# Performance work log

Hardware: AMD Instinct MI355X
Metric: run time of the kernel (lower is better)

The kernel has to match this reference:

```python
import jax, jax.numpy as jnp
import numpy as np

V, D, H, L, F, B, S = 512, 512, 8, 6, 2048, 8, 1024
DK = D // H
EPS = 1e-5


def _positional_encoding(max_len, d_model):
    pos = np.arange(max_len, dtype=np.float32)[:, None]
    div = np.exp(np.arange(0, d_model, 2, dtype=np.float32) * (-np.log(10000.0) / d_model))
    pe = np.zeros((max_len, d_model), dtype=np.float32)
    pe[:, 0::2] = np.sin(pos * div)
    pe[:, 1::2] = np.cos(pos * div)
    return jnp.asarray(pe)


def setup_inputs() -> dict:
    key = jax.random.key(0)
    ks = jax.random.split(key, 24)
    xavier = lambda k, shp: jax.random.normal(k, shp, jnp.float32) * np.sqrt(2.0 / (shp[-2] + shp[-1]))
    inp = {
        "input_ids": jax.random.randint(ks[0], (B, S), 0, V),
        "emb": jax.random.normal(ks[1], (V, D), jnp.float32) * 0.02,
        "pe": _positional_encoding(1024, D),
        "Wq": xavier(ks[2], (L, D, D)), "bq": jnp.zeros((L, D)),
        "Wk": xavier(ks[3], (L, D, D)), "bk": jnp.zeros((L, D)),
        "Wv": xavier(ks[4], (L, D, D)), "bv": jnp.zeros((L, D)),
        "Wo": xavier(ks[5], (L, D, D)), "bo": jnp.zeros((L, D)),
        "ln1_g": jnp.ones((L, D)), "ln1_b": jnp.zeros((L, D)),
        "W1": xavier(ks[6], (L, D, F)), "b1": jnp.zeros((L, F)),
        "W2": xavier(ks[7], (L, F, D)), "b2": jnp.zeros((L, D)),
        "ln2_g": jnp.ones((L, D)), "ln2_b": jnp.zeros((L, D)),
        "Wout": xavier(ks[8], (D, V)), "bout": jnp.zeros((V,)),
    }
    return inp


def _ln(x, g, b):
    mu = jnp.mean(x, -1, keepdims=True)
    var = jnp.mean(jnp.square(x - mu), -1, keepdims=True)
    return (x - mu) * jax.lax.rsqrt(var + EPS) * g + b


def reference(input_ids, emb, pe, Wq, bq, Wk, bk, Wv, bv, Wo, bo,
              ln1_g, ln1_b, W1, b1, W2, b2, ln2_g, ln2_b, Wout, bout):
    h = emb[input_ids] * np.sqrt(D) + pe[:S]  # [B,S,D]
    # Faithful to the original mask bug: masked_fill(mask==0, -1e9) fills the
    # LOWER triangle (incl diagonal); raw scores are kept strictly where j > i.
    r = jnp.arange(S)
    keep = r[None, :] > r[:, None]  # [S,S]

    def block(h, p):
        (wq, bq_, wk, bk_, wv, bv_, wo, bo_,
         g1, be1, w1, b1_, w2, b2_, g2, be2) = p
        split = lambda t: t.reshape(B, S, H, DK).transpose(0, 2, 1, 3)
        q = split(h @ wq + bq_)
        k = split(h @ wk + bk_)
        v = split(h @ wv + bv_)
        scores = jnp.einsum('bhqd,bhkd->bhqk', q, k) / np.sqrt(DK)
        scores = jnp.where(keep, scores, -1e9)
        a = jax.nn.softmax(scores, axis=-1)
        o = jnp.einsum('bhqk,bhkd->bhqd', a, v).transpose(0, 2, 1, 3).reshape(B, S, D)
        h = _ln(h + (o @ wo + bo_), g1, be1)
        f = jax.nn.relu(h @ w1 + b1_) @ w2 + b2_
        h = _ln(h + f, g2, be2)
        return h, None

    params = (Wq, bq, Wk, bk, Wv, bv, Wo, bo, ln1_g, ln1_b, W1, b1, W2, b2, ln2_g, ln2_b)
    h, _ = jax.lax.scan(block, h, params)
    return h @ Wout + bout  # logits [B,S,V]
```

## Files before the change

### kernel.cpp

```cpp
#include <hip/hip_runtime.h>

typedef unsigned short u16;
typedef __attribute__((ext_vector_type(8))) short bf16x8;
typedef __attribute__((ext_vector_type(4))) float f32x4;
typedef __attribute__((ext_vector_type(4))) unsigned int uint4v;
typedef __attribute__((ext_vector_type(4))) unsigned short us4;

#define NLAYER 6
#define D_MODEL 512
#define NHEAD 8
#define DKH 64
#define SEQ 1024
#define BATCH 8
#define FFN 2048
#define MROWS (BATCH * SEQ)
#define QKV_LD 1536
#define SCALE_LOG2E 0.18033688011112042f

__device__ __forceinline__ float b2f(u16 u) {
  union { unsigned u32; float f; } x; x.u32 = ((unsigned)u) << 16; return x.f;
}
__device__ __forceinline__ u16 f2b(float f) {
  union { float f; unsigned u; } x; x.f = f;
  unsigned r = x.u + 0x7FFFu + ((x.u >> 16) & 1u);
  return (u16)(r >> 16);
}
__device__ __forceinline__ void gld16(const u16* g, u16* l) {
  __builtin_amdgcn_global_load_lds(
      (const __attribute__((address_space(1))) unsigned int*)g,
      (__attribute__((address_space(3))) unsigned int*)l, 16, 0, 0);
}
__device__ __forceinline__ void barrier_raw() {
  asm volatile("" ::: "memory");
  __builtin_amdgcn_s_barrier();
  asm volatile("" ::: "memory");
}

__global__ __launch_bounds__(256) void transpose_cvt_kernel(
    const float* __restrict__ src, u16* __restrict__ dst, int K, int N, size_t dstZ,
    float scale)
{
  __shared__ float t[32][33];
  const int z = blockIdx.z;
  src += (size_t)z * K * N;
  dst += (size_t)z * dstZ;
  const int n0 = blockIdx.x * 32, k0 = blockIdx.y * 32;
  const int tx = threadIdx.x, ty = threadIdx.y;
#pragma unroll
  for (int i = 0; i < 32; i += 8)
    t[ty + i][tx] = src[(size_t)(k0 + ty + i) * N + n0 + tx];
  __syncthreads();
#pragma unroll
  for (int i = 0; i < 32; i += 8)
    dst[(size_t)(n0 + ty + i) * K + k0 + tx] = f2b(t[tx][ty + i] * scale);
}

__global__ __launch_bounds__(256) void concat_bias_kernel(
    const float* __restrict__ bq, const float* __restrict__ bk,
    const float* __restrict__ bv, float* __restrict__ dst)
{
  const int l = blockIdx.x, t = threadIdx.x;
#pragma unroll
  for (int j = t; j < 512; j += 256) {
    dst[l * QKV_LD + j]        = bq[l * 512 + j] * SCALE_LOG2E;
    dst[l * QKV_LD + 512 + j]  = bk[l * 512 + j];
    dst[l * QKV_LD + 1024 + j] = bv[l * 512 + j];
  }
}

__global__ __launch_bounds__(256) void embed_kernel(
    const int* __restrict__ ids, const float* __restrict__ emb,
    const float* __restrict__ pe, float* __restrict__ Hf, u16* __restrict__ Hb)
{
  const int row = blockIdx.x;
  const int s = row & (SEQ - 1);
  const int id = ids[row];
  const int tid = threadIdx.x;
#pragma unroll
  for (int u = 0; u < 2; ++u) {
    const int d = tid + u * 256;
    float v = emb[(size_t)id * D_MODEL + d] * 22.62741699796952f + pe[(size_t)s * D_MODEL + d];
    Hf[(size_t)row * D_MODEL + d] = v;
    Hb[(size_t)row * D_MODEL + d] = f2b(v);
  }
}

template<bool RELU, bool VT>
__global__ __launch_bounds__(512, 2) void gemm256_kernel(
    const u16* __restrict__ A, const u16* __restrict__ Bt,
    const float* __restrict__ bias,
    u16* __restrict__ Cb, u16* __restrict__ Vtp,
    int M, int N, int K)
{
  extern __shared__ __align__(16) u16 smem[];
  u16* Asm = smem;
  u16* Bsm = smem + 32768;
  const int tid = threadIdx.x;
  const int wave = tid >> 6, lane = tid & 63;
  const int lm = lane & 15, quad = lane >> 4, l7 = lm & 7;
  const int wm = wave >> 2, wn = wave & 3;
  const int bm = blockIdx.x * 256, bn = blockIdx.y * 256;

  const int srow = tid >> 3;
  const int scg = (tid & 7) ^ (srow & 7);
  const u16* Ap = A  + (size_t)(bm + srow) * K + scg * 8;
  const u16* Bp = Bt + (size_t)(bn + srow) * K + scg * 8;
  u16* uA = Asm + wave * 512;
  u16* uB = Bsm + wave * 512;

  f32x4 acc[8][4] = {};

  const int NT = K >> 6;
  auto stage = [&](int buf, int t) {
    const size_t ko = (size_t)t << 6;
#pragma unroll
    for (int p = 0; p < 4; ++p)
      gld16(Ap + (size_t)(p * 64) * K + ko, uA + buf * 16384 + p * 4096);
#pragma unroll
    for (int p = 0; p < 4; ++p)
      gld16(Bp + (size_t)(p * 64) * K + ko, uB + buf * 16384 + p * 4096);
  };

  stage(0, 0);
  __syncthreads();

  const int sl0 = (quad ^ l7) << 3;
  const int sl1 = ((quad + 4) ^ l7) << 3;

#pragma unroll 1
  for (int t = 0; t < NT; ++t) {
    const int cur = t & 1;
    if (t + 1 < NT) stage(cur ^ 1, t + 1);
    const u16* as_ = Asm + cur * 16384 + (wm * 128 + lm) * 64;
    const u16* bs_ = Bsm + cur * 16384 + (wn * 64 + lm) * 64;
    bf16x8 af[4][2], b01[2][2], b23[2][2];
#pragma unroll
    for (int i = 0; i < 4; ++i) {
      af[i][0] = *(const bf16x8*)&as_[i * 1024 + sl0];
      af[i][1] = *(const bf16x8*)&as_[i * 1024 + sl1];
    }
#pragma unroll
    for (int j = 0; j < 2; ++j) {
      b01[j][0] = *(const bf16x8*)&bs_[j * 1024 + sl0];
      b01[j][1] = *(const bf16x8*)&bs_[j * 1024 + sl1];
    }
    __builtin_amdgcn_s_setprio(1);
#pragma unroll
    for (int i = 0; i < 4; ++i)
#pragma unroll
      for (int j = 0; j < 2; ++j) {
        acc[i][j] = __builtin_amdgcn_mfma_f32_16x16x32_bf16(af[i][0], b01[j][0], acc[i][j], 0, 0, 0);
        acc[i][j] = __builtin_amdgcn_mfma_f32_16x16x32_bf16(af[i][1], b01[j][1], acc[i][j], 0, 0, 0);
      }
    __builtin_amdgcn_s_setprio(0);
    barrier_raw();
#pragma unroll
    for (int j = 0; j < 2; ++j) {
      b23[j][0] = *(const bf16x8*)&bs_[(j + 2) * 1024 + sl0];
      b23[j][1] = *(const bf16x8*)&bs_[(j + 2) * 1024 + sl1];
    }
    __builtin_amdgcn_s_setprio(1);
#pragma unroll
    for (int i = 0; i < 4; ++i)
#pragma unroll
      for (int j = 0; j < 2; ++j) {
        acc[i][j + 2] = __builtin_amdgcn_mfma_f32_16x16x32_bf16(af[i][0], b23[j][0], acc[i][j + 2], 0, 0, 0);
        acc[i][j + 2] = __builtin_amdgcn_mfma_f32_16x16x32_bf16(af[i][1], b23[j][1], acc[i][j + 2], 0, 0, 0);
      }
    __builtin_amdgcn_s_setprio(0);
    barrier_raw();
#pragma unroll
    for (int i = 0; i < 4; ++i) {
      af[i][0] = *(const bf16x8*)&as_[(i + 4) * 1024 + sl0];
      af[i][1] = *(const bf16x8*)&as_[(i + 4) * 1024 + sl1];
    }
    __builtin_amdgcn_s_setprio(1);
#pragma unroll
    for (int i = 0; i < 4; ++i)
#pragma unroll
      for (int j = 0; j < 2; ++j) {
        acc[i + 4][j + 2] = __builtin_amdgcn_mfma_f32_16x16x32_bf16(af[i][0], b23[j][0], acc[i + 4][j + 2], 0, 0, 0);
        acc[i + 4][j + 2] = __builtin_amdgcn_mfma_f32_16x16x32_bf16(af[i][1], b23[j][1], acc[i + 4][j + 2], 0, 0, 0);
      }
    __builtin_amdgcn_s_setprio(0);
    barrier_raw();
#pragma unroll
    for (int j = 0; j < 2; ++j) {
      b01[j][0] = *(const bf16x8*)&bs_[j * 1024 + sl0];
      b01[j][1] = *(const bf16x8*)&bs_[j * 1024 + sl1];
    }
    __builtin_amdgcn_s_setprio(1);
#pragma unroll
    for (int i = 0; i < 4; ++i)
#pragma unroll
      for (int j = 0; j < 2; ++j) {
        acc[i + 4][j] = __builtin_amdgcn_mfma_f32_16x16x32_bf16(af[i][0], b01[j][0], acc[i + 4][j], 0, 0, 0);
        acc[i + 4][j] = __builtin_amdgcn_mfma_f32_16x16x32_bf16(af[i][1], b01[j][1], acc[i + 4][j], 0, 0, 0);
      }
    __builtin_amdgcn_s_setprio(0);
    if (t + 1 < NT) {
      asm volatile("s_waitcnt vmcnt(0)" ::: "memory");
      barrier_raw();
    }
  }

  const int mbase = bm + wm * 128 + quad * 4;
  const int nbase = bn + wn * 64 + lm;
#pragma unroll
  for (int i = 0; i < 8; ++i) {
#pragma unroll
    for (int j = 0; j < 4; ++j) {
      const int n = nbase + j * 16;
      const float bv = bias[n];
      float vv[4];
#pragma unroll
      for (int r = 0; r < 4; ++r) {
        float v = acc[i][j][r] + bv;
        if (RELU) v = fmaxf(v, 0.f);
        vv[r] = v;
      }
      if (VT && n >= 1024) {
        const int hh = (n - 1024) >> 6, d = (n - 1024) & 63;
        const int mm = mbase + i * 16;
        const int bb = mm >> 10, ss = mm & 1023;
        us4 pk;
#pragma unroll
        for (int r = 0; r < 4; ++r) pk[r] = f2b(vv[r]);
        *(us4*)&Vtp[(((size_t)(bb * NHEAD + hh)) * 64 + d) * SEQ + ss] = pk;
      } else {
#pragma unroll
        for (int r = 0; r < 4; ++r) {
          const int m = mbase + i * 16 + r;
          Cb[(size_t)m * N + n] = f2b(vv[r]);
        }
      }
    }
  }
}

template<bool LN>
__global__ __launch_bounds__(512, 2) void gemm_ln_kernel(
    const u16* __restrict__ A, const u16* __restrict__ Bt,
    const float* __restrict__ bias,
    const float* __restrict__ gw, const float* __restrict__ bw,
    float* __restrict__ Hf, u16* __restrict__ Hb, float* __restrict__ Cf,
    int K)
{
  extern __shared__ __align__(16) u16 smem[];
  u16* Asm = smem;
  u16* Bsm = smem + 4096;
  float* red = (float*)(smem + 69632);
  const int tid = threadIdx.x;
  const int wave = tid >> 6, lane = tid & 63;
  const int lm = lane & 15, quad = lane >> 4, l7 = lm & 7;
  const int bm = blockIdx.x * 32;

  const int srow = tid >> 3;
  const int scg = (tid & 7) ^ (srow & 7);
  const u16* Ap = A  + (size_t)(bm + srow) * K + scg * 8;
  const u16* Bp = Bt + (size_t)srow * K + scg * 8;
  u16* uA = Asm + wave * 512;
  u16* uB = Bsm + wave * 512;

  f32x4 acc[2][4] = {};
  const int NT = K >> 6;
  auto stage = [&](int buf, int t) {
    const size_t ko = (size_t)t << 6;
    if (wave < 4) gld16(Ap + ko, uA + buf * 2048);
#pragma unroll
    for (int p = 0; p < 8; ++p)
      gld16(Bp + (size_t)(p * 64) * K + ko, uB + buf * 32768 + p * 4096);
  };

  stage(0, 0);
  __syncthreads();

#pragma unroll 1
  for (int t = 0; t < NT; ++t) {
    const int cur = t & 1;
    if (t + 1 < NT) stage(cur ^ 1, t + 1);
    const u16* as_ = Asm + cur * 2048 + lm * 64;
    const u16* bs_ = Bsm + cur * 32768 + (wave * 64 + lm) * 64;
#pragma unroll
    for (int kh = 0; kh < 2; ++kh) {
      const int slot = ((kh * 4 + quad) ^ l7) << 3;
      bf16x8 af[2], bg[4];
      af[0] = *(const bf16x8*)&as_[slot];
      af[1] = *(const bf16x8*)&as_[1024 + slot];
#pragma unroll
      for (int j = 0; j < 4; ++j)
        bg[j] = *(const bf16x8*)&bs_[j * 1024 + slot];
#pragma unroll
      for (int i = 0; i < 2; ++i)
#pragma unroll
        for (int j = 0; j < 4; ++j)
          acc[i][j] = __builtin_amdgcn_mfma_f32_16x16x32_bf16(af[i], bg[j], acc[i][j], 0, 0, 0);
    }
    __syncthreads();
  }

  const int col0 = wave * 64 + lm;
  float bi[4];
#pragma unroll
  for (int j = 0; j < 4; ++j) bi[j] = bias[col0 + j * 16];

  if (LN) {
    float gv[4], bv[4];
#pragma unroll
    for (int j = 0; j < 4; ++j) { gv[j] = gw[col0 + j * 16]; bv[j] = bw[col0 + j * 16]; }
    float x[2][4][4];
    float ps[8], pq[8];
#pragma unroll
    for (int k = 0; k < 8; ++k) { ps[k] = 0.f; pq[k] = 0.f; }
#pragma unroll
    for (int i = 0; i < 2; ++i)
#pragma unroll
      for (int r = 0; r < 4; ++r) {
        const int rowl = i * 16 + quad * 4 + r;
        const size_t rb = (size_t)(bm + rowl) * D_MODEL;
#pragma unroll
        for (int j = 0; j < 4; ++j) {
          float xv = acc[i][j][r] + bi[j] + Hf[rb + col0 + j * 16];
          x[i][j][r] = xv;
          ps[i * 4 + r] += xv;
          pq[i * 4 + r] += xv * xv;
        }
      }
#pragma unroll
    for (int o = 1; o < 16; o <<= 1)
#pragma unroll
      for (int k = 0; k < 8; ++k) {
        ps[k] += __shfl_xor(ps[k], o, 16);
        pq[k] += __shfl_xor(pq[k], o, 16);
      }
    if (lm == 0) {
#pragma unroll
      for (int k = 0; k < 8; ++k) {
        const int rowl = (k >> 2) * 16 + quad * 4 + (k & 3);
        red[wave * 32 + rowl] = ps[k];
        red[256 + wave * 32 + rowl] = pq[k];
      }
    }
    __syncthreads();
    if (tid < 32) {
      float s = 0.f, q = 0.f;
#pragma unroll
      for (int w = 0; w < 8; ++w) { s += red[w * 32 + tid]; q += red[256 + w * 32 + tid]; }
      const float mu = s * (1.f / 512.f);
      const float var = q * (1.f / 512.f) - mu * mu;
      red[512 + tid] = mu;
      red[544 + tid] = rsqrtf(var + 1e-5f);
    }
    __syncthreads();
#pragma unroll
    for (int i = 0; i < 2; ++i)
#pragma unroll
      for (int r = 0; r < 4; ++r) {
        const int rowl = i * 16 + quad * 4 + r;
        const float mu = red[512 + rowl];
        const float rs = red[544 + rowl];
        const size_t rb = (size_t)(bm + rowl) * D_MODEL;
#pragma unroll
        for (int j = 0; j < 4; ++j) {
          const float y = (x[i][j][r] - mu) * rs * gv[j] + bv[j];
          Hf[rb + col0 + j * 16] = y;
          Hb[rb + col0 + j * 16] = f2b(y);
        }
      }
  } else {
#pragma unroll
    for (int i = 0; i < 2; ++i)
#pragma unroll
      for (int r = 0; r < 4; ++r) {
        const int rowl = i * 16 + quad * 4 + r;
        const size_t rb = (size_t)(bm + rowl) * D_MODEL;
#pragma unroll
        for (int j = 0; j < 4; ++j)
          Cf[rb + col0 + j * 16] = acc[i][j][r] + bi[j];
      }
  }
}

__global__ __launch_bounds__(256) void attn_mfma_kernel(
    const u16* __restrict__ QKV, const u16* __restrict__ Vt, u16* __restrict__ O)
{
  __shared__ __align__(16) u16 Ks[64 * 64];
  __shared__ __align__(16) u16 Vs[64 * 64];
  __shared__ __align__(16) u16 Ps[4 * 16 * 64];
  const int tid = threadIdx.x;
  const int wave = tid >> 6, lane = tid & 63;
  const int quad = lane >> 4, l15 = lane & 15;
  const int l7 = l15 & 7;
  const int id = blockIdx.x;
  const int bh = id & 63;
  const int b = bh >> 3, h = bh & 7;
  const int g = id >> 6;
  const int u = g * 4 + wave;
  u16* psw = Ps + wave * (16 * 64);
  const size_t qoff = (size_t)b * SEQ * QKV_LD + h * 64;
  const size_t vtb  = (size_t)bh * 64 * SEQ;

  const int sr = tid >> 3, sc = tid & 7;
  const u16* kg0 = QKV + qoff + 512 + (size_t)sr * QKV_LD + sc * 8;
  const u16* kg1 = kg0 + (size_t)32 * QKV_LD;
  const u16* vg0 = Vt + vtb + (size_t)sr * SEQ + sc * 8;
  const u16* vg1 = vg0 + (size_t)32 * SEQ;
  const int sw = (sc ^ (sr & 7)) << 3;
  u16* ks0 = &Ks[sr * 64 + sw];
  u16* ks1 = &Ks[(sr + 32) * 64 + sw];
  u16* vs0 = &Vs[sr * 64 + sw];
  u16* vs1 = &Vs[(sr + 32) * 64 + sw];

  const u16* qp = QKV + qoff + (size_t)(u * 16 + l15) * QKV_LD + quad * 8;
  const bf16x8 qf0 = *(const bf16x8*)(qp);
  const bf16x8 qf1 = *(const bf16x8*)(qp + 32);

  f32x4 oacc[4] = {};
  float lsum[4] = {0.f, 0.f, 0.f, 0.f};

  uint4v kr0 = *(const uint4v*)(kg0 + (size_t)(g * 64) * QKV_LD);
  uint4v kr1 = *(const uint4v*)(kg1 + (size_t)(g * 64) * QKV_LD);
  uint4v vr0 = *(const uint4v*)(vg0 + g * 64);
  uint4v vr1 = *(const uint4v*)(vg1 + g * 64);

#pragma unroll 1
  for (int jt = g; jt < 16; ++jt) {
    __syncthreads();
    *(uint4v*)ks0 = kr0; *(uint4v*)ks1 = kr1;
    *(uint4v*)vs0 = vr0; *(uint4v*)vs1 = vr1;
    __syncthreads();
    if (jt < 15) {
      kr0 = *(const uint4v*)(kg0 + (size_t)((jt + 1) * 64) * QKV_LD);
      kr1 = *(const uint4v*)(kg1 + (size_t)((jt + 1) * 64) * QKV_LD);
      vr0 = *(const uint4v*)(vg0 + (jt + 1) * 64);
      vr1 = *(const uint4v*)(vg1 + (jt + 1) * 64);
    }
    f32x4 sacc[4] = {};
#pragma unroll
    for (int nt = 0; nt < 4; ++nt) {
      const int key = nt * 16 + l15, k7 = key & 7;
      bf16x8 kb0 = *(const bf16x8*)&Ks[key * 64 + ((quad ^ k7) << 3)];
      bf16x8 kb1 = *(const bf16x8*)&Ks[key * 64 + (((quad + 4) ^ k7) << 3)];
      sacc[nt] = __builtin_amdgcn_mfma_f32_16x16x32_bf16(qf0, kb0, sacc[nt], 0, 0, 0);
      sacc[nt] = __builtin_amdgcn_mfma_f32_16x16x32_bf16(qf1, kb1, sacc[nt], 0, 0, 0);
    }
    const bool diag = (jt == g);
#pragma unroll
    for (int nt = 0; nt < 4; ++nt)
#pragma unroll
      for (int r = 0; r < 4; ++r) {
        float pv = __builtin_amdgcn_exp2f(sacc[nt][r]);
        if (diag) {
          const int i = u * 16 + quad * 4 + r;
          const int j = jt * 64 + nt * 16 + l15;
          pv = (j > i) ? pv : 0.f;
        }
        lsum[r] += pv;
        const int qr = quad * 4 + r;
        const int j2 = nt * 16 + l15;
        psw[qr * 64 + (((j2 >> 3) ^ (qr & 7)) << 3) + (j2 & 7)] = f2b(pv);
      }
    bf16x8 pf0 = *(const bf16x8*)&psw[l15 * 64 + (((quad + 0) ^ l7) << 3)];
    bf16x8 pf1 = *(const bf16x8*)&psw[l15 * 64 + (((quad + 4) ^ l7) << 3)];
#pragma unroll
    for (int nt = 0; nt < 4; ++nt) {
      const int d = nt * 16 + l15, d7 = d & 7;
      bf16x8 vb0 = *(const bf16x8*)&Vs[d * 64 + ((quad ^ d7) << 3)];
      bf16x8 vb1 = *(const bf16x8*)&Vs[d * 64 + (((quad + 4) ^ d7) << 3)];
      oacc[nt] = __builtin_amdgcn_mfma_f32_16x16x32_bf16(pf0, vb0, oacc[nt], 0, 0, 0);
      oacc[nt] = __builtin_amdgcn_mfma_f32_16x16x32_bf16(pf1, vb1, oacc[nt], 0, 0, 0);
    }
  }

#pragma unroll
  for (int o = 1; o < 16; o <<= 1)
#pragma unroll
    for (int r = 0; r < 4; ++r) lsum[r] += __shfl_xor(lsum[r], o, 16);
  float rl[4];
#pragma unroll
  for (int r = 0; r < 4; ++r) rl[r] = 1.0f / lsum[r];
#pragma unroll
  for (int nt = 0; nt < 4; ++nt)
#pragma unroll
    for (int r = 0; r < 4; ++r) {
      const int row = u * 16 + quad * 4 + r;
      O[(size_t)(b * SEQ + row) * D_MODEL + h * DKH + nt * 16 + l15] = f2b(oacc[nt][r] * rl[r]);
    }

  if (g == 15) {
    __syncthreads();
    const int d = tid >> 2, scv = (tid & 3) * 256;
    const u16* pv = Vt + vtb + (size_t)d * SEQ + scv;
    float s = 0.f;
#pragma unroll 8
    for (int i2 = 0; i2 < 256; ++i2) s += b2f(pv[i2]);
    s += __shfl_xor(s, 1, 64);
    s += __shfl_xor(s, 2, 64);
    if ((tid & 3) == 0)
      O[((size_t)b * SEQ + SEQ - 1) * D_MODEL + h * 64 + d] = f2b(s * (1.f / SEQ));
  }
}

extern "C" void kernel_launch(void* const* d_in, const int* in_sizes, int n_in,
                              void* d_out, int out_size, void* d_ws, size_t ws_size,
                              hipStream_t stream) {
  (void)in_sizes; (void)n_in; (void)out_size; (void)ws_size;
  const int*   ids  = (const int*)  d_in[0];
  const float* emb  = (const float*)d_in[1];
  const float* pe   = (const float*)d_in[2];
  const float* Wq   = (const float*)d_in[3];
  const float* bq   = (const float*)d_in[4];
  const float* Wk   = (const float*)d_in[5];
  const float* bk   = (const float*)d_in[6];
  const float* Wv   = (const float*)d_in[7];
  const float* bv   = (const float*)d_in[8];
  const float* Wo   = (const float*)d_in[9];
  const float* bo   = (const float*)d_in[10];
  const float* g1   = (const float*)d_in[11];
  const float* be1  = (const float*)d_in[12];
  const float* W1   = (const float*)d_in[13];
  const float* b1   = (const float*)d_in[14];
  const float* W2   = (const float*)d_in[15];
  const float* b2   = (const float*)d_in[16];
  const float* g2   = (const float*)d_in[17];
  const float* be2  = (const float*)d_in[18];
  const float* Wout = (const float*)d_in[19];
  const float* bout = (const float*)d_in[20];
  float* out = (float*)d_out;

  static int attr_set = 0;
  if (!attr_set) {
    hipFuncSetAttribute(reinterpret_cast<const void*>(&gemm256_kernel<false, true>),
                        hipFuncAttributeMaxDynamicSharedMemorySize, 131072);
    hipFuncSetAttribute(reinterpret_cast<const void*>(&gemm256_kernel<true, false>),
                        hipFuncAttributeMaxDynamicSharedMemorySize, 131072);
    hipFuncSetAttribute(reinterpret_cast<const void*>(&gemm_ln_kernel<true>),
                        hipFuncAttributeMaxDynamicSharedMemorySize, 141568);
    hipFuncSetAttribute(reinterpret_cast<const void*>(&gemm_ln_kernel<false>),
                        hipFuncAttributeMaxDynamicSharedMemorySize, 141568);
    attr_set = 1;
  }

  char* wsp = (char*)d_ws;
  auto alloc = [&](size_t bytes) -> char* {
    char* p = wsp; wsp += (bytes + 255) & ~(size_t)255; return p;
  };
  const size_t dd  = (size_t)D_MODEL * D_MODEL;
  const size_t df  = (size_t)D_MODEL * FFN;
  const size_t dq  = (size_t)QKV_LD * D_MODEL;
  u16* wqkv_t = (u16*)alloc(NLAYER * dq * 2);
  u16* wo_t   = (u16*)alloc(NLAYER * dd * 2);
  u16* w1_t   = (u16*)alloc(NLAYER * df * 2);
  u16* w2_t   = (u16*)alloc(NLAYER * df * 2);
  u16* wout_t = (u16*)alloc(dd * 2);
  float* bqkv = (float*)alloc(NLAYER * QKV_LD * 4);
  float* hf   = (float*)alloc((size_t)MROWS * D_MODEL * 4);
  u16*   hb   = (u16*)  alloc((size_t)MROWS * D_MODEL * 2);
  u16*   qkvb = (u16*)  alloc((size_t)MROWS * QKV_LD * 2);
  u16*   ob   = (u16*)  alloc((size_t)MROWS * D_MODEL * 2);
  u16*   vt   = (u16*)  alloc((size_t)BATCH * NHEAD * DKH * SEQ * 2);
  u16*   mid  = qkvb;

  dim3 tb8(32, 8);
  transpose_cvt_kernel<<<dim3(16, 16, NLAYER), tb8, 0, stream>>>(Wq, wqkv_t,            512, 512,  dq, SCALE_LOG2E);
  transpose_cvt_kernel<<<dim3(16, 16, NLAYER), tb8, 0, stream>>>(Wk, wqkv_t + 512*512,  512, 512,  dq, 1.f);
  transpose_cvt_kernel<<<dim3(16, 16, NLAYER), tb8, 0, stream>>>(Wv, wqkv_t + 1024*512, 512, 512,  dq, 1.f);
  transpose_cvt_kernel<<<dim3(16, 16, NLAYER), tb8, 0, stream>>>(Wo, wo_t,   512, 512,  dd, 1.f);
  transpose_cvt_kernel<<<dim3(64, 16, NLAYER), tb8, 0, stream>>>(W1, w1_t,   512, 2048, df, 1.f);
  transpose_cvt_kernel<<<dim3(16, 64, NLAYER), tb8, 0, stream>>>(W2, w2_t,   2048, 512, df, 1.f);
  transpose_cvt_kernel<<<dim3(16, 16, 1),      tb8, 0, stream>>>(Wout, wout_t, 512, 512, dd, 1.f);
  concat_bias_kernel<<<NLAYER, 256, 0, stream>>>(bq, bk, bv, bqkv);

  embed_kernel<<<MROWS, 256, 0, stream>>>(ids, emb, pe, hf, hb);

  for (int l = 0; l < NLAYER; ++l) {
    gemm256_kernel<false, true><<<dim3(32, 6), 512, 131072, stream>>>(
        hb, wqkv_t + l * dq, bqkv + l * QKV_LD, qkvb, vt, MROWS, QKV_LD, 512);
    attn_mfma_kernel<<<1024, 256, 0, stream>>>(qkvb, vt, ob);
    gemm_ln_kernel<true><<<256, 512, 141568, stream>>>(
        ob, wo_t + l * dd, bo + l * 512, g1 + l * 512, be1 + l * 512,
        hf, hb, nullptr, 512);
    gemm256_kernel<true, false><<<dim3(32, 8), 512, 131072, stream>>>(
        hb, w1_t + l * df, b1 + l * 2048, mid, nullptr, MROWS, 2048, 512);
    gemm_ln_kernel<true><<<256, 512, 141568, stream>>>(
        mid, w2_t + l * df, b2 + l * 512, g2 + l * 512, be2 + l * 512,
        hf, hb, nullptr, 2048);
  }
  gemm_ln_kernel<false><<<256, 512, 141568, stream>>>(
      hb, wout_t, bout, nullptr, nullptr, nullptr, nullptr, out, 512);
}
```

Baseline: 991.3 us.

## Use 4-stage cp.async-style pipeline with K=32 tiles in gemm_ln kernel

Reworks the gemm_ln main loop from a double-buffered K=64 tile with a __syncthreads per iteration to a four-buffer ring of K=32 tiles with three tiles prefetched ahead. Explicit vmcnt waits plus a raw barrier replace the full sync, so global loads for future tiles stay in flight while the current tile is computed. Swizzle and load mapping change to match the narrower tile. The cost is more barriers per unit of K and hand-tuned waitcnt values that depend on each wave's exact load count.

```diff
diff --git a/kernel.cpp b/kernel.cpp
--- a/kernel.cpp
+++ b/kernel.cpp
@@ -252,51 +252,53 @@
   float* red = (float*)(smem + 69632);
   const int tid = threadIdx.x;
   const int wave = tid >> 6, lane = tid & 63;
-  const int lm = lane & 15, quad = lane >> 4, l7 = lm & 7;
+  const int lm = lane & 15, quad = lane >> 4;
   const int bm = blockIdx.x * 32;
 
-  const int srow = tid >> 3;
-  const int scg = (tid & 7) ^ (srow & 7);
-  const u16* Ap = A  + (size_t)(bm + srow) * K + scg * 8;
-  const u16* Bp = Bt + (size_t)srow * K + scg * 8;
-  u16* uA = Asm + wave * 512;
-  u16* uB = Bsm + wave * 512;
+  const int sr = tid >> 2;
+  const int sc = (tid & 3) ^ (sr & 3);
+  const u16* Bp = Bt + (size_t)sr * K + sc * 8;
+  const u16* Ap = A + (size_t)(bm + sr) * K + sc * 8;
 
   f32x4 acc[2][4] = {};
-  const int NT = K >> 6;
+  const int NT = K >> 5;
   auto stage = [&](int buf, int t) {
-    const size_t ko = (size_t)t << 6;
-    if (wave < 4) gld16(Ap + ko, uA + buf * 2048);
-#pragma unroll
-    for (int p = 0; p < 8; ++p)
-      gld16(Bp + (size_t)(p * 64) * K + ko, uB + buf * 32768 + p * 4096);
+    const size_t ko = (size_t)t << 5;
+#pragma unroll
+    for (int p = 0; p < 4; ++p)
+      gld16(Bp + (size_t)(p * 128) * K + ko, Bsm + buf * 16384 + p * 4096 + wave * 512);
+    if (wave < 2) gld16(Ap + ko, Asm + buf * 1024 + wave * 512);
   };
 
   stage(0, 0);
-  __syncthreads();
+  if (NT > 1) stage(1, 1);
+  if (NT > 2) stage(2, 2);
+
+  const int sl = (quad ^ (lm & 3)) << 3;
 
 #pragma unroll 1
   for (int t = 0; t < NT; ++t) {
-    const int cur = t & 1;
-    if (t + 1 < NT) stage(cur ^ 1, t + 1);
-    const u16* as_ = Asm + cur * 2048 + lm * 64;
-    const u16* bs_ = Bsm + cur * 32768 + (wave * 64 + lm) * 64;
-#pragma unroll
-    for (int kh = 0; kh < 2; ++kh) {
-      const int slot = ((kh * 4 + quad) ^ l7) << 3;
-      bf16x8 af[2], bg[4];
-      af[0] = *(const bf16x8*)&as_[slot];
-      af[1] = *(const bf16x8*)&as_[1024 + slot];
-#pragma unroll
-      for (int j = 0; j < 4; ++j)
-        bg[j] = *(const bf16x8*)&bs_[j * 1024 + slot];
-#pragma unroll
-      for (int i = 0; i < 2; ++i)
-#pragma unroll
-        for (int j = 0; j < 4; ++j)
-          acc[i][j] = __builtin_amdgcn_mfma_f32_16x16x32_bf16(af[i], bg[j], acc[i][j], 0, 0, 0);
-    }
-    __syncthreads();
+    if (t + 3 <= NT) {
+      if (wave < 2) asm volatile("s_waitcnt vmcnt(10)" ::: "memory");
+      else          asm volatile("s_waitcnt vmcnt(8)"  ::: "memory");
+    } else {
+      asm volatile("s_waitcnt vmcnt(0)" ::: "memory");
+    }
+    barrier_raw();
+    if (t + 3 < NT) stage((t + 3) & 3, t + 3);
+    const u16* as_ = Asm + (t & 3) * 1024 + lm * 32;
+    const u16* bs_ = Bsm + (t & 3) * 16384 + (wave * 64 + lm) * 32;
+    bf16x8 af0 = *(const bf16x8*)&as_[sl];
+    bf16x8 af1 = *(const bf16x8*)&as_[512 + sl];
+    bf16x8 bg[4];
+#pragma unroll
+    for (int j = 0; j < 4; ++j)
+      bg[j] = *(const bf16x8*)&bs_[j * 512 + sl];
+#pragma unroll
+    for (int j = 0; j < 4; ++j) {
+      acc[0][j] = __builtin_amdgcn_mfma_f32_16x16x32_bf16(af0, bg[j], acc[0][j], 0, 0, 0);
+      acc[1][j] = __builtin_amdgcn_mfma_f32_16x16x32_bf16(af1, bg[j], acc[1][j], 0, 0, 0);
+    }
   }
 
   const int col0 = wave * 64 + lm;
```

After: 1.032 ms. 4.1% more time.

## Split FFN down-projection into tiled GEMM plus separate add-LayerNorm kernel

Applied to the files above, without the earlier changes.

Replaces the fused GEMM+LayerNorm kernel for the W2 projection (K=2048), which ran only 256 blocks, with a generic 64x128-tiled GEMM using 512 blocks that writes a bf16 intermediate. A separate per-row kernel then does the residual add and LayerNorm. The aim is more parallelism and better occupancy for the long-K GEMM. The cost is an extra launch, an extra bf16 round trip through global memory, and an added rounding of the FFN output before the residual.

```diff
diff --git a/kernel.cpp b/kernel.cpp
--- a/kernel.cpp
+++ b/kernel.cpp
@@ -82,6 +82,109 @@
     float v = emb[(size_t)id * D_MODEL + d] * 22.62741699796952f + pe[(size_t)s * D_MODEL + d];
     Hf[(size_t)row * D_MODEL + d] = v;
     Hb[(size_t)row * D_MODEL + d] = f2b(v);
+  }
+}
+
+template<int BMT, bool RELU, bool OUTF, bool OUTB, bool VT>
+__global__ __launch_bounds__(256) void gemm_kernel(
+    const u16* __restrict__ A, const u16* __restrict__ Bt,
+    const float* __restrict__ bias,
+    float* __restrict__ Cf, u16* __restrict__ Cb, u16* __restrict__ Vtp,
+    int M, int N, int K)
+{
+  constexpr int IT = BMT / 32;
+  constexpr int AHALF = BMT * 64;
+  constexpr int BHALF = 128 * 64;
+  __shared__ __align__(16) u16 As[2 * AHALF];
+  __shared__ __align__(16) u16 Bs[2 * BHALF];
+  const int tid = threadIdx.x;
+  const int bm = blockIdx.x * BMT, bn = blockIdx.y * 128;
+  const int wave = tid >> 6, lane = tid & 63;
+  const int lm = lane & 15, quad = lane >> 4;
+  const int wm = (wave & 1) * (BMT / 2), wn = (wave >> 1) * 64;
+
+  const int sr = tid >> 3;
+  const int sc = (tid & 7) ^ (sr & 7);
+  const u16* Ap = A  + (size_t)(bm + sr) * K + sc * 8;
+  const u16* Bp = Bt + (size_t)(bn + sr) * K + sc * 8;
+  u16* lA = As + wave * 512;
+  u16* lB = Bs + wave * 512;
+
+  f32x4 acc[IT][4] = {};
+
+  const int nt = K >> 6;
+  auto stage = [&](int buf, int t) {
+    const size_t ko = (size_t)t << 6;
+#pragma unroll
+    for (int p = 0; p < BMT / 32; ++p)
+      gld16(Ap + (size_t)(p * 32) * K + ko, lA + buf * AHALF + p * 2048);
+#pragma unroll
+    for (int p = 0; p < 4; ++p)
+      gld16(Bp + (size_t)(p * 32) * K + ko, lB + buf * BHALF + p * 2048);
+  };
+
+  stage(0, 0);
+  __syncthreads();
+
+  for (int t = 0; t < nt; ++t) {
+    const int cur = t & 1;
+    if (t + 1 < nt) stage(cur ^ 1, t + 1);
+    const u16* as = As + cur * AHALF;
+    const u16* bs = Bs + cur * BHALF;
+#pragma unroll
+    for (int kh = 0; kh < 2; ++kh) {
+      bf16x8 af[IT], bg[4];
+#pragma unroll
+      for (int i = 0; i < IT; ++i) {
+        const int row = wm + i * 16 + lm;
+        af[i] = *(const bf16x8*)&as[row * 64 + (((kh * 4 + quad) ^ (row & 7)) << 3)];
+      }
+#pragma unroll
+      for (int j = 0; j < 4; ++j) {
+        const int row = wn + j * 16 + lm;
+        bg[j] = *(const bf16x8*)&bs[row * 64 + (((kh * 4 + quad) ^ (row & 7)) << 3)];
+      }
+#pragma unroll
+      for (int i = 0; i < IT; ++i)
+#pragma unroll
+        for (int j = 0; j < 4; ++j)
+          acc[i][j] = __builtin_amdgcn_mfma_f32_16x16x32_bf16(af[i], bg[j], acc[i][j], 0, 0, 0);
+    }
+    __syncthreads();
+  }
+
+  const int mbase = bm + wm + quad * 4;
+  const int nbase = bn + wn + lm;
+#pragma unroll
+  for (int i = 0; i < IT; ++i) {
+#pragma unroll
+    for (int j = 0; j < 4; ++j) {
+      const int n = nbase + j * 16;
+      const float bv = bias[n];
+      float vv[4];
+#pragma unroll
+      for (int r = 0; r < 4; ++r) {
+        float v = acc[i][j][r] + bv;
+        if (RELU) v = fmaxf(v, 0.f);
+        vv[r] = v;
+      }
+      if (VT && n >= 1024) {
+        const int hh = (n - 1024) >> 6, d = (n - 1024) & 63;
+        const int mm = mbase + i * 16;
+        const int bb = mm >> 10, ss = mm & 1023;
+        us4 pk;
+#pragma unroll
+        for (int r = 0; r < 4; ++r) pk[r] = f2b(vv[r]);
+        *(us4*)&Vtp[(((size_t)(bb * NHEAD + hh)) * 64 + d) * SEQ + ss] = pk;
+      } else {
+#pragma unroll
+        for (int r = 0; r < 4; ++r) {
+          const int m = mbase + i * 16 + r;
+          if (OUTF) Cf[(size_t)m * N + n] = vv[r];
+          if (OUTB) Cb[(size_t)m * N + n] = f2b(vv[r]);
+        }
+      }
+    }
   }
 }
 
@@ -499,6 +602,39 @@
     if ((tid & 3) == 0)
       O[((size_t)b * SEQ + SEQ - 1) * D_MODEL + h * 64 + d] = f2b(s * (1.f / SEQ));
   }
+}
+
+__global__ __launch_bounds__(256) void add_ln_kernel(
+    const float* __restrict__ Hin, const u16* __restrict__ T,
+    const float* __restrict__ g, const float* __restrict__ bta,
+    float* __restrict__ Hout, u16* __restrict__ Hb)
+{
+  __shared__ float red[8];
+  const int row = blockIdx.x, tid = threadIdx.x;
+  const int wave = tid >> 6, lane = tid & 63;
+  const size_t base = (size_t)row * D_MODEL;
+  const float x0 = Hin[base + tid] + b2f(T[base + tid]);
+  const float x1 = Hin[base + tid + 256] + b2f(T[base + tid + 256]);
+  float s = x0 + x1;
+#pragma unroll
+  for (int o = 32; o > 0; o >>= 1) s += __shfl_xor(s, o, 64);
+  if (lane == 0) red[wave] = s;
+  __syncthreads();
+  const float mu = (red[0] + red[1] + red[2] + red[3]) * (1.f / 512.f);
+  const float d0 = x0 - mu, d1 = x1 - mu;
+  float v = d0 * d0 + d1 * d1;
+#pragma unroll
+  for (int o = 32; o > 0; o >>= 1) v += __shfl_xor(v, o, 64);
+  if (lane == 0) red[4 + wave] = v;
+  __syncthreads();
+  const float var = (red[4] + red[5] + red[6] + red[7]) * (1.f / 512.f);
+  const float rs = rsqrtf(var + 1e-5f);
+  const float y0 = d0 * rs * g[tid] + bta[tid];
+  const float y1 = d1 * rs * g[tid + 256] + bta[tid + 256];
+  Hout[base + tid] = y0;
+  Hout[base + tid + 256] = y1;
+  Hb[base + tid] = f2b(y0);
+  Hb[base + tid + 256] = f2b(y1);
 }
 
 extern "C" void kernel_launch(void* const* d_in, const int* in_sizes, int n_in,
@@ -559,6 +695,7 @@
   u16*   qkvb = (u16*)  alloc((size_t)MROWS * QKV_LD * 2);
   u16*   ob   = (u16*)  alloc((size_t)MROWS * D_MODEL * 2);
   u16*   vt   = (u16*)  alloc((size_t)BATCH * NHEAD * DKH * SEQ * 2);
+  u16*   tb   = (u16*)  alloc((size_t)MROWS * D_MODEL * 2);
   u16*   mid  = qkvb;
 
   dim3 tb8(32, 8);
@@ -582,9 +719,9 @@
         hf, hb, nullptr, 512);
     gemm256_kernel<true, false><<<dim3(32, 8), 512, 131072, stream>>>(
         hb, w1_t + l * df, b1 + l * 2048, mid, nullptr, MROWS, 2048, 512);
-    gemm_ln_kernel<true><<<256, 512, 141568, stream>>>(
-        mid, w2_t + l * df, b2 + l * 512, g2 + l * 512, be2 + l * 512,
-        hf, hb, nullptr, 2048);
+    gemm_kernel<64, false, false, true, false><<<dim3(128, 4), 256, 0, stream>>>(
+        mid, w2_t + l * df, b2 + l * 512, nullptr, tb, nullptr, MROWS, 512, 2048);
+    add_ln_kernel<<<MROWS, 256, 0, stream>>>(hf, tb, g2 + l * 512, be2 + l * 512, hf, hb);
   }
   gemm_ln_kernel<false><<<256, 512, 141568, stream>>>(
       hb, wout_t, bout, nullptr, nullptr, nullptr, nullptr, out, 512);
```

Result: faster. 969.2 us (-2.2%).
